# Performance work log

Measured on AMD Instinct MI355X. Metric: run time of the kernel, lower is better.

## Reference

```python
import jax, jax.numpy as jnp
import numpy as np

B, S, D, H = 4, 2048, 1024, 16
HD = D // H
DFF = 4 * D
EPS = 1e-5


def setup_inputs() -> dict:
    key = jax.random.key(0)
    ks = jax.random.split(key, 8)
    s = 0.02
    return {
        "x": jax.random.normal(ks[0], (B, S, D), dtype=jnp.float32),
        "ln1_g": jnp.ones((D,), jnp.float32),
        "ln1_b": jnp.zeros((D,), jnp.float32),
        "Wq": jax.random.normal(ks[1], (D, D), jnp.float32) * s,
        "Wk": jax.random.normal(ks[2], (D, D), jnp.float32) * s,
        "Wv": jax.random.normal(ks[3], (D, D), jnp.float32) * s,
        "Wo": jax.random.normal(ks[4], (D, D), jnp.float32) * s,
        "ln2_g": jnp.ones((D,), jnp.float32),
        "ln2_b": jnp.zeros((D,), jnp.float32),
        "W1": jax.random.normal(ks[5], (D, DFF), jnp.float32) * s,
        "b1": jnp.zeros((DFF,), jnp.float32),
        "W2": jax.random.normal(ks[6], (DFF, D), jnp.float32) * s,
        "b2": jnp.zeros((D,), jnp.float32),
    }


def _layernorm(x, g, b):
    mu = jnp.mean(x, axis=-1, keepdims=True)
    var = jnp.var(x, axis=-1, keepdims=True)
    return (x - mu) * jax.lax.rsqrt(var + EPS) * g + b


def _block(x, ln1_g, ln1_b, Wq, Wk, Wv, Wo, ln2_g, ln2_b, W1, b1, W2, b2):
    # --- attention sub-block (pre-norm) ---
    h = _layernorm(x, ln1_g, ln1_b)
    q = (h @ Wq).reshape(B, S, H, HD)
    k = (h @ Wk).reshape(B, S, H, HD)
    v = (h @ Wv).reshape(B, S, H, HD)
    scores = jnp.einsum("bqhd,bkhd->bhqk", q, k) / np.sqrt(HD).astype(np.float32)
    causal = jnp.tril(jnp.ones((S, S), dtype=bool))
    scores = jnp.where(causal, scores, -jnp.inf)
    attn = jax.nn.softmax(scores, axis=-1)  # dropout p=0 (eval)
    ctx = jnp.einsum("bhqk,bkhd->bqhd", attn, v).reshape(B, S, D)
    x = x + ctx @ Wo
    # --- FFN sub-block (pre-norm) ---
    h = _layernorm(x, ln2_g, ln2_b)
    h = jax.nn.gelu(h @ W1 + b1, approximate=False)  # torch nn.GELU() = exact erf
    return x + (h @ W2 + b2)


def reference(x, ln1_g, ln1_b, Wq, Wk, Wv, Wo, ln2_g, ln2_b, W1, b1, W2, b2):
    return _block(x, ln1_g, ln1_b, Wq, Wk, Wv, Wo, ln2_g, ln2_b, W1, b1, W2, b2)
```

## Files before the change

### kernel.cpp

```cpp
#include <hip/hip_runtime.h>
#include <hip/hip_bf16.h>
#include <math.h>

#define NB 4
#define NS 2048
#define ND 1024
#define NH 16
#define NHD 64
#define NDFF 4096
#define QKS 3072

typedef __attribute__((ext_vector_type(8))) short bf16x8;
typedef __attribute__((ext_vector_type(4))) float f32x4;
typedef __attribute__((ext_vector_type(16))) float f32x16;
typedef __attribute__((ext_vector_type(4))) short short4v;
typedef __attribute__((ext_vector_type(4))) int i32x4;

static __device__ __forceinline__ short f2b(float f) {
  union { __hip_bfloat16 b; short s; } u;
  u.b = __float2bfloat16(f);
  return u.s;
}

static __device__ __forceinline__ int cvtpk(float lo, float hi_) {
  int r;
  asm("v_cvt_pk_bf16_f32 %0, %1, %2" : "=v"(r) : "v"(lo), "v"(hi_));
  return r;
}

static __device__ __forceinline__ float pairmax(float x) {
  auto r = __builtin_amdgcn_permlane32_swap(__float_as_uint(x), __float_as_uint(x), false, false);
  return fmaxf(__uint_as_float(r[0]), __uint_as_float(r[1]));
}
static __device__ __forceinline__ float pairsum(float x) {
  auto r = __builtin_amdgcn_permlane32_swap(__float_as_uint(x), __float_as_uint(x), false, false);
  return __uint_as_float(r[0]) + __uint_as_float(r[1]);
}

__global__ __launch_bounds__(256) void ln_kernel(
    const float* __restrict__ x, const float* __restrict__ g,
    const float* __restrict__ b, short* __restrict__ out) {
  __shared__ float red[8];
  const int row = blockIdx.x;
  const int t = threadIdx.x;
  const float* xr = x + (size_t)row * ND;
  const float4 xv = *(const float4*)(xr + t * 4);
  float s = xv.x + xv.y + xv.z + xv.w;
  float ss = xv.x * xv.x + xv.y * xv.y + xv.z * xv.z + xv.w * xv.w;
#pragma unroll
  for (int m = 32; m >= 1; m >>= 1) {
    s += __shfl_xor(s, m);
    ss += __shfl_xor(ss, m);
  }
  if ((t & 63) == 0) { red[(t >> 6) * 2] = s; red[(t >> 6) * 2 + 1] = ss; }
  __syncthreads();
  s = red[0] + red[2] + red[4] + red[6];
  ss = red[1] + red[3] + red[5] + red[7];
  const float mu = s * (1.0f / ND);
  const float var = ss * (1.0f / ND) - mu * mu;
  const float rs = rsqrtf(var + 1e-5f);
  const float4 gv = *(const float4*)(g + t * 4);
  const float4 bv = *(const float4*)(b + t * 4);
  short o[4];
  o[0] = f2b((xv.x - mu) * rs * gv.x + bv.x);
  o[1] = f2b((xv.y - mu) * rs * gv.y + bv.y);
  o[2] = f2b((xv.z - mu) * rs * gv.z + bv.z);
  o[3] = f2b((xv.w - mu) * rs * gv.w + bv.w);
  *(short4v*)(out + (size_t)row * ND + t * 4) = *(short4v*)o;
}

__global__ __launch_bounds__(256) void tcast_kernel(
    const float* __restrict__ in, short* __restrict__ out, int K, int N) {
  __shared__ float tile[32][33];
  const int n0 = blockIdx.x * 32, k0 = blockIdx.y * 32;
  const int tx = threadIdx.x & 31, ty = threadIdx.x >> 5;
#pragma unroll
  for (int i = 0; i < 32; i += 8)
    tile[ty + i][tx] = in[(size_t)(k0 + ty + i) * N + n0 + tx];
  __syncthreads();
#pragma unroll
  for (int i = 0; i < 32; i += 8)
    out[(size_t)(n0 + ty + i) * K + k0 + tx] = f2b(tile[tx][ty + i]);
}

__global__ __launch_bounds__(256) void vtrans_kernel(
    const short* __restrict__ in, short* __restrict__ out) {
  __shared__ short tile[64][72];
  const int s0 = blockIdx.x * 64, bh = blockIdx.y;
  const int bb = bh >> 4, hh = bh & 15;
  const int rr = threadIdx.x >> 3, cc = (threadIdx.x & 7) * 8;
#pragma unroll
  for (int it = 0; it < 2; ++it) {
    const int r = rr + it * 32;
    *(bf16x8*)&tile[r][cc] =
        *(const bf16x8*)&in[((size_t)(bb * NS + s0 + r)) * QKS + 2048 + hh * NHD + cc];
  }
  __syncthreads();
  const size_t ob = (size_t)bh * NHD * NS;
#pragma unroll
  for (int it = 0; it < 2; ++it) {
    const int d = rr + it * 32;
    short o[8];
#pragma unroll
    for (int j = 0; j < 8; ++j) o[j] = tile[cc + j][d];
    *(bf16x8*)&out[ob + (size_t)d * NS + s0 + cc] = *(bf16x8*)o;
  }
}

__device__ __forceinline__ void gload16(const void* g, void* l) {
  __builtin_amdgcn_global_load_lds(
      (const __attribute__((address_space(1))) unsigned int*)g,
      (__attribute__((address_space(3))) unsigned int*)l, 16, 0, 0);
}

template <int EPI>
__global__ __launch_bounds__(256, 3) void gemm97_kernel(
    const short* __restrict__ A, const short* __restrict__ Bt,
    float* __restrict__ Cf, short* __restrict__ Cb,
    const float* __restrict__ bias, const float* __restrict__ res,
    int M, int N, int K) {
  __shared__ short lds[2 * 128 * 64];
  const int tid = threadIdx.x, l = tid & 63, w = tid >> 6;
  const int wm = w >> 1, wn = w & 1;
  const int nbm = M >> 7, nbn = N >> 7, nwg = nbm * nbn;
  int wg = blockIdx.x;
  wg = (wg & 7) * (nwg >> 3) + (wg >> 3);
  const int bm = wg / nbn, bn = wg % nbn;

  const int srow = tid >> 3;
  const int sslot = (tid & 7) ^ (srow & 7);
  const short* Asrc = A + (size_t)(bm * 128 + srow) * K + sslot * 8;
  const short* Bsrc = Bt + (size_t)(bn * 128 + srow) * K + sslot * 8;
  const int wdst = w * 512;

  const int fr = l & 15, fg4 = l >> 4;
  int arow[4], brow[4];
#pragma unroll
  for (int i = 0; i < 4; ++i) {
    arow[i] = wm * 64 + i * 16 + fr;
    brow[i] = wn * 64 + i * 16 + fr;
  }

  f32x4 acc[4][4] = {};
  const int NT = K >> 6;

#pragma unroll
  for (int j = 0; j < 4; ++j) {
    gload16(Asrc, &lds[j * 2048 + wdst]);
    gload16(Bsrc, &lds[8192 + j * 2048 + wdst]);
    Asrc += (size_t)32 * K;
    Bsrc += (size_t)32 * K;
  }
  Asrc -= (size_t)128 * K;
  Bsrc -= (size_t)128 * K;

  for (int t = 0; t < NT; ++t) {
    __syncthreads();
#pragma unroll
    for (int kh = 0; kh < 2; ++kh) {
      bf16x8 af[4], bf[4];
#pragma unroll
      for (int i = 0; i < 4; ++i) {
        af[i] = *(const bf16x8*)&lds[arow[i] * 64 + (((kh * 4 + fg4) ^ (arow[i] & 7)) << 3)];
        bf[i] = *(const bf16x8*)&lds[8192 + brow[i] * 64 + (((kh * 4 + fg4) ^ (brow[i] & 7)) << 3)];
      }
      __builtin_amdgcn_s_setprio(1);
#pragma unroll
      for (int mi = 0; mi < 4; ++mi)
#pragma unroll
        for (int ni = 0; ni < 4; ++ni)
          acc[mi][ni] = __builtin_amdgcn_mfma_f32_16x16x32_bf16(af[mi], bf[ni], acc[mi][ni], 0, 0, 0);
      __builtin_amdgcn_s_setprio(0);
    }
    __syncthreads();
    if (t + 1 < NT) {
      const short* a = Asrc + (size_t)(t + 1) * 64;
      const short* b = Bsrc + (size_t)(t + 1) * 64;
#pragma unroll
      for (int j = 0; j < 4; ++j) {
        gload16(a, &lds[j * 2048 + wdst]);
        gload16(b, &lds[8192 + j * 2048 + wdst]);
        a += (size_t)32 * K;
        b += (size_t)32 * K;
      }
    }
  }

  const int fq = (l >> 4) * 4;
  const int wrb = bm * 128 + wm * 64;
  const int wcb = bn * 128 + wn * 64;
#pragma unroll
  for (int mi = 0; mi < 4; ++mi) {
#pragma unroll
    for (int ni = 0; ni < 4; ++ni) {
#pragma unroll
      for (int rr = 0; rr < 4; ++rr) {
        const int row = wrb + mi * 16 + fq + rr;
        const int col = wcb + ni * 16 + fr;
        float v = acc[mi][ni][rr];
        if (EPI == 0) {
          Cb[(size_t)row * N + col] = f2b(v);
        } else if (EPI == 1) {
          Cf[(size_t)row * N + col] = v + res[(size_t)row * N + col];
        } else if (EPI == 2) {
          v += bias[col];
          v = 0.5f * v * (1.0f + erff(v * 0.70710678118f));
          Cb[(size_t)row * N + col] = f2b(v);
        } else {
          Cf[(size_t)row * N + col] = v + bias[col] + res[(size_t)row * N + col];
        }
      }
    }
  }
}

__global__ __launch_bounds__(256, 2) void attn_kernel(
    const short* __restrict__ qkv, const short* __restrict__ vt, short* __restrict__ ctx) {
  __shared__ short Kls[2][64 * 64];
  __shared__ short Vls[2][64 * 64];

  const int bid = blockIdx.x;
  const int bh = (bid & 7) * 8 + ((bid >> 3) & 7);
  const int cp = bid >> 6;
  const int bb = bh >> 4, hh = bh & 15;
  const int lane = threadIdx.x & 63, wave = threadIdx.x >> 6;
  const int ql = lane & 31, hi = lane >> 5;
  const int qbA = cp * 128 + wave * 32;
  const int qbB = (15 - cp) * 128 + wave * 32;

  bf16x8 qf[2][4];
#pragma unroll
  for (int hf = 0; hf < 2; ++hf) {
    const int qb0 = hf ? qbB : qbA;
    const size_t qrow = ((size_t)bb * NS + qb0 + ql) * QKS + hh * NHD;
#pragma unroll
    for (int st = 0; st < 4; ++st)
      qf[hf][st] = *(const bf16x8*)&qkv[qrow + st * 16 + hi * 8];
  }

  f32x16 acc[2][2] = {};
  float m_run[2] = {-1e37f, -1e37f};
  float l_run[2] = {0.f, 0.f};

  const int srow = lane >> 3;
  const int sslot = (lane & 7) ^ srow;
  const short* kbasep = qkv + (size_t)bb * NS * QKS + 1024 + hh * NHD + sslot * 8;
  const short* vbasep = vt + (size_t)bh * NHD * NS + sslot * 8;

  const int nkt = (16 - cp) * 2;
#pragma unroll
  for (int r = 0; r < 2; ++r) {
    const int row = r * 32 + wave * 8 + srow;
    gload16(kbasep + (size_t)row * QKS, &Kls[0][(r * 32 + wave * 8) * 64]);
    gload16(vbasep + (size_t)row * NS, &Vls[0][(r * 32 + wave * 8) * 64]);
  }

  int buf = 0;
  for (int jt = 0; jt < nkt; ++jt) {
    asm volatile("s_waitcnt vmcnt(0)\n\ts_barrier" ::: "memory");
    if (jt + 1 < nkt) {
      const int k0n = (jt + 1) * 64;
#pragma unroll
      for (int r = 0; r < 2; ++r) {
        const int row = r * 32 + wave * 8 + srow;
        gload16(kbasep + (size_t)(k0n + row) * QKS, &Kls[buf ^ 1][(r * 32 + wave * 8) * 64]);
        gload16(vbasep + (size_t)row * NS + k0n, &Vls[buf ^ 1][(r * 32 + wave * 8) * 64]);
      }
    }
    const int k0 = jt * 64;
    const short* Kb = &Kls[buf][0];
    const short* Vb = &Vls[buf][0];
#pragma unroll
    for (int ks = 0; ks < 2; ++ks) {
      const int kbase = k0 + ks * 32;
      if (kbase > qbB) continue;
      bf16x8 kf[4], vf[2][2];
      const int krow = ks * 32 + ql;
#pragma unroll
      for (int st = 0; st < 4; ++st)
        kf[st] = *(const bf16x8*)&Kb[krow * 64 + ((st * 2 + hi) ^ (krow & 7)) * 8];
#pragma unroll
      for (int db = 0; db < 2; ++db) {
        const int vrow = db * 32 + ql;
#pragma unroll
        for (int su = 0; su < 2; ++su)
          vf[db][su] =
              *(const bf16x8*)&Vb[vrow * 64 + ((ks * 4 + su * 2 + hi) ^ (vrow & 7)) * 8];
      }
#pragma unroll
      for (int hf = 0; hf < 2; ++hf) {
        const int qb0 = hf ? qbB : qbA;
        if (kbase > qb0) continue;
        const int qg = qb0 + ql;
        f32x16 s = {};
        __builtin_amdgcn_s_setprio(1);
#pragma unroll
        for (int st = 0; st < 4; ++st)
          s = __builtin_amdgcn_mfma_f32_32x32x16_bf16(kf[st], qf[hf][st], s, 0, 0, 0);
        __builtin_amdgcn_s_setprio(0);
        const bool masked = (kbase + 31 > qb0);
        float pv[16];
        float mt = -INFINITY;
#pragma unroll
        for (int r = 0; r < 16; ++r) {
          float v = s[r] * 0.125f;
          if (masked) {
            const int key = kbase + 4 * hi + (r & 3) + 8 * (r >> 2);
            v = (key > qg) ? -INFINITY : v;
          }
          pv[r] = v;
          mt = fmaxf(mt, v);
        }
        mt = pairmax(mt);
        if (!__all(mt - m_run[hf] <= 8.0f)) {
          const float mn = fmaxf(m_run[hf], mt);
          const float sc = __expf(m_run[hf] - mn);
          m_run[hf] = mn;
          l_run[hf] *= sc;
          acc[hf][0] *= sc;
          acc[hf][1] *= sc;
        }
        float pe[16];
        float lt = 0.f;
#pragma unroll
        for (int r = 0; r < 16; ++r) {
          pe[r] = __expf(fminf(pv[r] - m_run[hf], 80.0f));
          lt += pe[r];
        }
        l_run[hf] += pairsum(lt);
        bf16x8 pf[2];
#pragma unroll
        for (int su = 0; su < 2; ++su) {
          const int a0 = cvtpk(pe[su * 8 + 0], pe[su * 8 + 1]);
          const int a1 = cvtpk(pe[su * 8 + 2], pe[su * 8 + 3]);
          const int b0 = cvtpk(pe[su * 8 + 4], pe[su * 8 + 5]);
          const int b1 = cvtpk(pe[su * 8 + 6], pe[su * 8 + 7]);
          auto r0 = __builtin_amdgcn_permlane32_swap((unsigned)a0, (unsigned)b0, false, false);
          auto r1 = __builtin_amdgcn_permlane32_swap((unsigned)a1, (unsigned)b1, false, false);
          union { i32x4 w; bf16x8 v; } u;
          u.w[0] = r0[0]; u.w[1] = r1[0]; u.w[2] = r0[1]; u.w[3] = r1[1];
          pf[su] = u.v;
        }
        __builtin_amdgcn_s_setprio(1);
#pragma unroll
        for (int su = 0; su < 2; ++su) {
          acc[hf][0] = __builtin_amdgcn_mfma_f32_32x32x16_bf16(vf[0][su], pf[su], acc[hf][0], 0, 0, 0);
          acc[hf][1] = __builtin_amdgcn_mfma_f32_32x32x16_bf16(vf[1][su], pf[su], acc[hf][1], 0, 0, 0);
        }
        __builtin_amdgcn_s_setprio(0);
      }
    }
    asm volatile("s_waitcnt lgkmcnt(0)\n\ts_barrier" ::: "memory");
    buf ^= 1;
  }

#pragma unroll
  for (int hf = 0; hf < 2; ++hf) {
    const int qb0 = hf ? qbB : qbA;
    const float inv = 1.0f / l_run[hf];
    const size_t ob = ((size_t)bb * NS + qb0 + ql) * ND + hh * NHD + hi * 8;
#pragma unroll
    for (int db = 0; db < 2; ++db) {
#pragma unroll
      for (int J = 0; J < 2; ++J) {
        const int a0 = cvtpk(acc[hf][db][J * 8 + 0] * inv, acc[hf][db][J * 8 + 1] * inv);
        const int a1 = cvtpk(acc[hf][db][J * 8 + 2] * inv, acc[hf][db][J * 8 + 3] * inv);
        const int b0 = cvtpk(acc[hf][db][J * 8 + 4] * inv, acc[hf][db][J * 8 + 5] * inv);
        const int b1 = cvtpk(acc[hf][db][J * 8 + 6] * inv, acc[hf][db][J * 8 + 7] * inv);
        auto r0 = __builtin_amdgcn_permlane32_swap((unsigned)a0, (unsigned)b0, false, false);
        auto r1 = __builtin_amdgcn_permlane32_swap((unsigned)a1, (unsigned)b1, false, false);
        union { i32x4 w; bf16x8 v; } u;
        u.w[0] = r0[0]; u.w[1] = r1[0]; u.w[2] = r0[1]; u.w[3] = r1[1];
        *(bf16x8*)&ctx[ob + db * 32 + J * 16] = u.v;
      }
    }
  }
}

extern "C" void kernel_launch(void* const* d_in, const int* in_sizes, int n_in,
                              void* d_out, int out_size, void* d_ws, size_t ws_size,
                              hipStream_t stream) {
  (void)in_sizes; (void)n_in; (void)out_size; (void)ws_size;
  const float* x     = (const float*)d_in[0];
  const float* ln1_g = (const float*)d_in[1];
  const float* ln1_b = (const float*)d_in[2];
  const float* Wq    = (const float*)d_in[3];
  const float* Wk    = (const float*)d_in[4];
  const float* Wv    = (const float*)d_in[5];
  const float* Wo    = (const float*)d_in[6];
  const float* ln2_g = (const float*)d_in[7];
  const float* ln2_b = (const float*)d_in[8];
  const float* W1    = (const float*)d_in[9];
  const float* b1    = (const float*)d_in[10];
  const float* W2    = (const float*)d_in[11];
  const float* b2    = (const float*)d_in[12];
  float* out = (float*)d_out;

  char* ws = (char*)d_ws;
  const size_t MiB = 1024 * 1024;
  short* wqkvT = (short*)(ws + 0 * MiB);
  short* woT   = (short*)(ws + 6 * MiB);
  short* w1T   = (short*)(ws + 8 * MiB);
  short* w2T   = (short*)(ws + 16 * MiB);
  short* h     = (short*)(ws + 24 * MiB);
  short* ctx   = (short*)(ws + 24 * MiB);
  short* qkv   = (short*)(ws + 40 * MiB);
  short* vt    = (short*)(ws + 88 * MiB);
  short* hff   = (short*)(ws + 40 * MiB);
  float* x1    = (float*)(ws + 104 * MiB);

  tcast_kernel<<<dim3(32, 32), 256, 0, stream>>>(Wq, wqkvT, 1024, 1024);
  tcast_kernel<<<dim3(32, 32), 256, 0, stream>>>(Wk, wqkvT + 1024 * 1024, 1024, 1024);
  tcast_kernel<<<dim3(32, 32), 256, 0, stream>>>(Wv, wqkvT + 2048 * 1024, 1024, 1024);
  tcast_kernel<<<dim3(32, 32), 256, 0, stream>>>(Wo, woT, 1024, 1024);
  tcast_kernel<<<dim3(128, 32), 256, 0, stream>>>(W1, w1T, 1024, 4096);
  tcast_kernel<<<dim3(32, 128), 256, 0, stream>>>(W2, w2T, 4096, 1024);

  ln_kernel<<<8192, 256, 0, stream>>>(x, ln1_g, ln1_b, h);

  gemm97_kernel<0><<<1536, 256, 0, stream>>>(h, wqkvT, nullptr, qkv, nullptr, nullptr,
                                             8192, 3072, 1024);
  vtrans_kernel<<<dim3(32, 64), 256, 0, stream>>>(qkv, vt);

  attn_kernel<<<512, 256, 0, stream>>>(qkv, vt, ctx);

  gemm97_kernel<1><<<512, 256, 0, stream>>>(ctx, woT, x1, nullptr, nullptr, x,
                                            8192, 1024, 1024);

  ln_kernel<<<8192, 256, 0, stream>>>(x1, ln2_g, ln2_b, h);

  gemm97_kernel<2><<<2048, 256, 0, stream>>>(h, w1T, nullptr, hff, b1, nullptr,
                                             8192, 4096, 1024);
  gemm97_kernel<3><<<512, 256, 0, stream>>>(hff, w2T, out, nullptr, b2, x1,
                                            8192, 1024, 4096);
}
```

Baseline: 364.8 us.

## Double-buffer GEMM LDS with BK=32 stages and prefetch next tile before compute

The GEMM kernel now uses two LDS buffers of 128x32 K-slices instead of one 128x64 buffer. The next tile's async global-to-LDS loads are issued at the top of each iteration, so they overlap the MFMA work on the current buffer, and the second barrier is removed. The launch bound rises to 4 waves-per-EU occupancy, and the swizzle is adapted to 32-wide rows. The trade-off is twice as many loop iterations and barriers per K. It also relies on a single barrier being enough to protect buffer reuse, and it is not obvious that the async LDS loads are fully waited on before use.

After: 380.7 us. 1.04x slower.

```diff
diff --git a/kernel.cpp b/kernel.cpp
--- a/kernel.cpp
+++ b/kernel.cpp
@@ -114,12 +114,12 @@
 }
 
 template <int EPI>
-__global__ __launch_bounds__(256, 3) void gemm97_kernel(
+__global__ __launch_bounds__(256, 4) void gemmd_kernel(
     const short* __restrict__ A, const short* __restrict__ Bt,
     float* __restrict__ Cf, short* __restrict__ Cb,
     const float* __restrict__ bias, const float* __restrict__ res,
     int M, int N, int K) {
-  __shared__ short lds[2 * 128 * 64];
+  __shared__ short lds[2][2 * 128 * 32];
   const int tid = threadIdx.x, l = tid & 63, w = tid >> 6;
   const int wm = w >> 1, wn = w & 1;
   const int nbm = M >> 7, nbn = N >> 7, nwg = nbm * nbn;
@@ -127,63 +127,52 @@
   wg = (wg & 7) * (nwg >> 3) + (wg >> 3);
   const int bm = wg / nbn, bn = wg % nbn;
 
-  const int srow = tid >> 3;
-  const int sslot = (tid & 7) ^ (srow & 7);
+  const int srow = tid >> 2;
+  const int sslot = (tid & 3) ^ ((srow >> 1) & 3);
   const short* Asrc = A + (size_t)(bm * 128 + srow) * K + sslot * 8;
   const short* Bsrc = Bt + (size_t)(bn * 128 + srow) * K + sslot * 8;
   const int wdst = w * 512;
 
   const int fr = l & 15, fg4 = l >> 4;
-  int arow[4], brow[4];
+  int aoff[4], boff[4];
 #pragma unroll
   for (int i = 0; i < 4; ++i) {
-    arow[i] = wm * 64 + i * 16 + fr;
-    brow[i] = wn * 64 + i * 16 + fr;
-  }
+    const int ra = wm * 64 + i * 16 + fr;
+    const int rb = wn * 64 + i * 16 + fr;
+    aoff[i] = ra * 32 + ((fg4 ^ ((ra >> 1) & 3)) << 3);
+    boff[i] = 4096 + rb * 32 + ((fg4 ^ ((rb >> 1) & 3)) << 3);
+  }
+
+  auto stage = [&](int t, int bsel) {
+    short* d = &lds[bsel][0];
+    const short* a = Asrc + (size_t)t * 32;
+    const short* b = Bsrc + (size_t)t * 32;
+    gload16(a, d + wdst);
+    gload16(a + (size_t)64 * K, d + 2048 + wdst);
+    gload16(b, d + 4096 + wdst);
+    gload16(b + (size_t)64 * K, d + 6144 + wdst);
+  };
 
   f32x4 acc[4][4] = {};
-  const int NT = K >> 6;
-
-#pragma unroll
-  for (int j = 0; j < 4; ++j) {
-    gload16(Asrc, &lds[j * 2048 + wdst]);
-    gload16(Bsrc, &lds[8192 + j * 2048 + wdst]);
-    Asrc += (size_t)32 * K;
-    Bsrc += (size_t)32 * K;
-  }
-  Asrc -= (size_t)128 * K;
-  Bsrc -= (size_t)128 * K;
-
+  const int NT = K >> 5;
+  stage(0, 0);
   for (int t = 0; t < NT; ++t) {
     __syncthreads();
-#pragma unroll
-    for (int kh = 0; kh < 2; ++kh) {
-      bf16x8 af[4], bf[4];
-#pragma unroll
-      for (int i = 0; i < 4; ++i) {
-        af[i] = *(const bf16x8*)&lds[arow[i] * 64 + (((kh * 4 + fg4) ^ (arow[i] & 7)) << 3)];
-        bf[i] = *(const bf16x8*)&lds[8192 + brow[i] * 64 + (((kh * 4 + fg4) ^ (brow[i] & 7)) << 3)];
-      }
-      __builtin_amdgcn_s_setprio(1);
-#pragma unroll
-      for (int mi = 0; mi < 4; ++mi)
-#pragma unroll
-        for (int ni = 0; ni < 4; ++ni)
-          acc[mi][ni] = __builtin_amdgcn_mfma_f32_16x16x32_bf16(af[mi], bf[ni], acc[mi][ni], 0, 0, 0);
-      __builtin_amdgcn_s_setprio(0);
+    if (t + 1 < NT) stage(t + 1, (t + 1) & 1);
+    const short* cur = &lds[t & 1][0];
+    bf16x8 af[4], bf[4];
+#pragma unroll
+    for (int i = 0; i < 4; ++i) {
+      af[i] = *(const bf16x8*)(cur + aoff[i]);
+      bf[i] = *(const bf16x8*)(cur + boff[i]);
     }
-    __syncthreads();
-    if (t + 1 < NT) {
-      const short* a = Asrc + (size_t)(t + 1) * 64;
-      const short* b = Bsrc + (size_t)(t + 1) * 64;
-#pragma unroll
-      for (int j = 0; j < 4; ++j) {
-        gload16(a, &lds[j * 2048 + wdst]);
-        gload16(b, &lds[8192 + j * 2048 + wdst]);
-        a += (size_t)32 * K;
-        b += (size_t)32 * K;
-      }
-    }
+    __builtin_amdgcn_s_setprio(1);
+#pragma unroll
+    for (int mi = 0; mi < 4; ++mi)
+#pragma unroll
+      for (int ni = 0; ni < 4; ++ni)
+        acc[mi][ni] = __builtin_amdgcn_mfma_f32_16x16x32_bf16(af[mi], bf[ni], acc[mi][ni], 0, 0, 0);
+    __builtin_amdgcn_s_setprio(0);
   }
 
   const int fq = (l >> 4) * 4;
@@ -418,19 +407,19 @@
 
   ln_kernel<<<8192, 256, 0, stream>>>(x, ln1_g, ln1_b, h);
 
-  gemm97_kernel<0><<<1536, 256, 0, stream>>>(h, wqkvT, nullptr, qkv, nullptr, nullptr,
-                                             8192, 3072, 1024);
+  gemmd_kernel<0><<<1536, 256, 0, stream>>>(h, wqkvT, nullptr, qkv, nullptr, nullptr,
+                                            8192, 3072, 1024);
   vtrans_kernel<<<dim3(32, 64), 256, 0, stream>>>(qkv, vt);
 
   attn_kernel<<<512, 256, 0, stream>>>(qkv, vt, ctx);
 
-  gemm97_kernel<1><<<512, 256, 0, stream>>>(ctx, woT, x1, nullptr, nullptr, x,
-                                            8192, 1024, 1024);
+  gemmd_kernel<1><<<512, 256, 0, stream>>>(ctx, woT, x1, nullptr, nullptr, x,
+                                           8192, 1024, 1024);
 
   ln_kernel<<<8192, 256, 0, stream>>>(x1, ln2_g, ln2_b, h);
 
-  gemm97_kernel<2><<<2048, 256, 0, stream>>>(h, w1T, nullptr, hff, b1, nullptr,
-                                             8192, 4096, 1024);
-  gemm97_kernel<3><<<512, 256, 0, stream>>>(hff, w2T, out, nullptr, b2, x1,
-                                            8192, 1024, 4096);
-}
+  gemmd_kernel<2><<<2048, 256, 0, stream>>>(h, w1T, nullptr, hff, b1, nullptr,
+                                            8192, 4096, 1024);
+  gemmd_kernel<3><<<512, 256, 0, stream>>>(hff, w2T, out, nullptr, b2, x1,
+                                           8192, 1024, 4096);
+}
```

## Group GEMM tiles for cache locality and store residual x1 as bf16

Applied to the files above, without the earlier changes.

Replaces the linear tile-to-block mapping in the GEMMs with a grouped GMxGN super-tile order, chosen per GEMM, so that concurrently running blocks share A and B panels in L2/MALL. The post-attention residual x1 is now written as bf16 instead of fp32, and the second layernorm and the final GEMM epilogue read that bf16 copy. This halves the traffic for that intermediate. The cost is precision: the residual stream x1 gets rounded to bf16, which can push the final output error toward the tolerance.

After: 359.3 us. Within noise of the previous version (-1.5%).

```diff
diff --git a/kernel.cpp b/kernel.cpp
--- a/kernel.cpp
+++ b/kernel.cpp
@@ -21,6 +21,11 @@
   u.b = __float2bfloat16(f);
   return u.s;
 }
+static __device__ __forceinline__ float b2f(short s) {
+  union { float f; unsigned u; } v;
+  v.u = ((unsigned)(unsigned short)s) << 16;
+  return v.f;
+}
 
 static __device__ __forceinline__ int cvtpk(float lo, float hi_) {
   int r;
@@ -37,16 +42,24 @@
   return __uint_as_float(r[0]) + __uint_as_float(r[1]);
 }
 
+template <bool BF16IN>
 __global__ __launch_bounds__(256) void ln_kernel(
-    const float* __restrict__ x, const float* __restrict__ g,
+    const void* __restrict__ xin, const float* __restrict__ g,
     const float* __restrict__ b, short* __restrict__ out) {
   __shared__ float red[8];
   const int row = blockIdx.x;
   const int t = threadIdx.x;
-  const float* xr = x + (size_t)row * ND;
-  const float4 xv = *(const float4*)(xr + t * 4);
-  float s = xv.x + xv.y + xv.z + xv.w;
-  float ss = xv.x * xv.x + xv.y * xv.y + xv.z * xv.z + xv.w * xv.w;
+  float xv[4];
+  if (BF16IN) {
+    const short4v sv = *(const short4v*)((const short*)xin + (size_t)row * ND + t * 4);
+#pragma unroll
+    for (int i = 0; i < 4; ++i) xv[i] = b2f(sv[i]);
+  } else {
+    const float4 fv = *(const float4*)((const float*)xin + (size_t)row * ND + t * 4);
+    xv[0] = fv.x; xv[1] = fv.y; xv[2] = fv.z; xv[3] = fv.w;
+  }
+  float s = xv[0] + xv[1] + xv[2] + xv[3];
+  float ss = xv[0] * xv[0] + xv[1] * xv[1] + xv[2] * xv[2] + xv[3] * xv[3];
 #pragma unroll
   for (int m = 32; m >= 1; m >>= 1) {
     s += __shfl_xor(s, m);
@@ -62,10 +75,10 @@
   const float4 gv = *(const float4*)(g + t * 4);
   const float4 bv = *(const float4*)(b + t * 4);
   short o[4];
-  o[0] = f2b((xv.x - mu) * rs * gv.x + bv.x);
-  o[1] = f2b((xv.y - mu) * rs * gv.y + bv.y);
-  o[2] = f2b((xv.z - mu) * rs * gv.z + bv.z);
-  o[3] = f2b((xv.w - mu) * rs * gv.w + bv.w);
+  o[0] = f2b((xv[0] - mu) * rs * gv.x + bv.x);
+  o[1] = f2b((xv[1] - mu) * rs * gv.y + bv.y);
+  o[2] = f2b((xv[2] - mu) * rs * gv.z + bv.z);
+  o[3] = f2b((xv[3] - mu) * rs * gv.w + bv.w);
   *(short4v*)(out + (size_t)row * ND + t * 4) = *(short4v*)o;
 }
 
@@ -113,19 +126,22 @@
       (__attribute__((address_space(3))) unsigned int*)l, 16, 0, 0);
 }
 
-template <int EPI>
-__global__ __launch_bounds__(256, 3) void gemm97_kernel(
+template <int GM, int GN, int EPI>
+__global__ __launch_bounds__(256, 3) void gemms_kernel(
     const short* __restrict__ A, const short* __restrict__ Bt,
     float* __restrict__ Cf, short* __restrict__ Cb,
-    const float* __restrict__ bias, const float* __restrict__ res,
-    int M, int N, int K) {
+    const float* __restrict__ bias, const float* __restrict__ resf,
+    const short* __restrict__ resb, int M, int N, int K) {
   __shared__ short lds[2 * 128 * 64];
   const int tid = threadIdx.x, l = tid & 63, w = tid >> 6;
   const int wm = w >> 1, wn = w & 1;
   const int nbm = M >> 7, nbn = N >> 7, nwg = nbm * nbn;
   int wg = blockIdx.x;
   wg = (wg & 7) * (nwg >> 3) + (wg >> 3);
-  const int bm = wg / nbn, bn = wg % nbn;
+  const int gidx = wg / (GM * GN), r = wg % (GM * GN);
+  const int ngn = nbn / GN;
+  const int bm = (gidx / ngn) * GM + r / GN;
+  const int bn = (gidx % ngn) * GN + r % GN;
 
   const int srow = tid >> 3;
   const int sslot = (tid & 7) ^ (srow & 7);
@@ -201,13 +217,13 @@
         if (EPI == 0) {
           Cb[(size_t)row * N + col] = f2b(v);
         } else if (EPI == 1) {
-          Cf[(size_t)row * N + col] = v + res[(size_t)row * N + col];
+          Cb[(size_t)row * N + col] = f2b(v + resf[(size_t)row * N + col]);
         } else if (EPI == 2) {
           v += bias[col];
           v = 0.5f * v * (1.0f + erff(v * 0.70710678118f));
           Cb[(size_t)row * N + col] = f2b(v);
         } else {
-          Cf[(size_t)row * N + col] = v + bias[col] + res[(size_t)row * N + col];
+          Cf[(size_t)row * N + col] = v + bias[col] + b2f(resb[(size_t)row * N + col]);
         }
       }
     }
@@ -407,7 +423,7 @@
   short* qkv   = (short*)(ws + 40 * MiB);
   short* vt    = (short*)(ws + 88 * MiB);
   short* hff   = (short*)(ws + 40 * MiB);
-  float* x1    = (float*)(ws + 104 * MiB);
+  short* x1b   = (short*)(ws + 104 * MiB);
 
   tcast_kernel<<<dim3(32, 32), 256, 0, stream>>>(Wq, wqkvT, 1024, 1024);
   tcast_kernel<<<dim3(32, 32), 256, 0, stream>>>(Wk, wqkvT + 1024 * 1024, 1024, 1024);
@@ -416,21 +432,21 @@
   tcast_kernel<<<dim3(128, 32), 256, 0, stream>>>(W1, w1T, 1024, 4096);
   tcast_kernel<<<dim3(32, 128), 256, 0, stream>>>(W2, w2T, 4096, 1024);
 
-  ln_kernel<<<8192, 256, 0, stream>>>(x, ln1_g, ln1_b, h);
-
-  gemm97_kernel<0><<<1536, 256, 0, stream>>>(h, wqkvT, nullptr, qkv, nullptr, nullptr,
-                                             8192, 3072, 1024);
+  ln_kernel<false><<<8192, 256, 0, stream>>>(x, ln1_g, ln1_b, h);
+
+  gemms_kernel<4, 6, 0><<<1536, 256, 0, stream>>>(h, wqkvT, nullptr, qkv, nullptr,
+                                                  nullptr, nullptr, 8192, 3072, 1024);
   vtrans_kernel<<<dim3(32, 64), 256, 0, stream>>>(qkv, vt);
 
   attn_kernel<<<512, 256, 0, stream>>>(qkv, vt, ctx);
 
-  gemm97_kernel<1><<<512, 256, 0, stream>>>(ctx, woT, x1, nullptr, nullptr, x,
-                                            8192, 1024, 1024);
-
-  ln_kernel<<<8192, 256, 0, stream>>>(x1, ln2_g, ln2_b, h);
-
-  gemm97_kernel<2><<<2048, 256, 0, stream>>>(h, w1T, nullptr, hff, b1, nullptr,
-                                             8192, 4096, 1024);
-  gemm97_kernel<3><<<512, 256, 0, stream>>>(hff, w2T, out, nullptr, b2, x1,
-                                            8192, 1024, 4096);
-}
+  gemms_kernel<4, 8, 1><<<512, 256, 0, stream>>>(ctx, woT, nullptr, x1b, nullptr,
+                                                 x, nullptr, 8192, 1024, 1024);
+
+  ln_kernel<true><<<8192, 256, 0, stream>>>(x1b, ln2_g, ln2_b, h);
+
+  gemms_kernel<4, 8, 2><<<2048, 256, 0, stream>>>(h, w1T, nullptr, hff, b1,
+                                                  nullptr, nullptr, 8192, 4096, 1024);
+  gemms_kernel<2, 2, 3><<<512, 256, 0, stream>>>(hff, w2T, out, nullptr, b2,
+                                                 nullptr, x1b, 8192, 1024, 4096);
+}
```
